# Kernel optimization log

Measured on AMD Instinct MI355X. Metric: run time of the kernel, lower is better.

## Reference

```python
import jax, jax.numpy as jnp
import numpy as np

# DCRNN (PEMS-BAY scale) constants
N = 325      # num_nodes
B = 64       # batch_size
T = 12       # encoder seq_len
HZ = 12      # decoder horizon
U = 64       # rnn_units
DIN = 2      # input_dim
DOUT = 1     # output_dim
K = 2        # max_diffusion_step
NM = K + 1   # num diffusion matrices (Chebyshev, single laplacian support)


def _glorot(key, shape):
    lim = float(np.sqrt(6.0 / (shape[0] + shape[1])))
    return jax.random.uniform(key, shape, jnp.float32, -lim, lim)


def setup_inputs() -> dict:
    key = jax.random.key(0)
    ks = jax.random.split(key, 8)
    # random symmetric adjacency -> scaled Laplacian support (lambda_max ~= 2 approx)
    a = np.asarray(jax.random.uniform(ks[0], (N, N)))
    a = (a + a.T) * 0.5
    a = a * (a > 0.9)
    d = a.sum(1)
    dinv = 1.0 / np.sqrt(np.maximum(d, 1e-8))
    L = np.eye(N, dtype=np.float32) - (dinv[:, None] * a * dinv[None, :]).astype(np.float32)
    support = jnp.asarray(L - np.eye(N, dtype=np.float32))  # 2L/lambda_max - I with lambda_max=2

    def cell_params(k, din):
        f = (din + U) * NM
        k1, k2 = jax.random.split(k)
        return dict(gate_W=_glorot(k1, (f, 2 * U)), gate_b=jnp.zeros((2 * U,), jnp.float32),
                    cand_W=_glorot(k2, (f, U)), cand_b=jnp.zeros((U,), jnp.float32))

    inp = {"inputs": jax.random.normal(ks[1], (T, B, N * DIN), jnp.float32),
           "support": support}
    for name, din, kk in [("enc0", DIN, ks[2]), ("enc1", U, ks[3]),
                          ("dec0", DOUT, ks[4]), ("dec1", U, ks[5])]:
        for pn, v in cell_params(kk, din).items():
            inp[f"{name}_{pn}"] = v
    inp["proj_W"] = _glorot(ks[6], (U, DOUT))
    inp["proj_b"] = jnp.zeros((DOUT,), jnp.float32)
    return inp


def _gconv(x, support, W, b):
    # x: (B, N, F). Chebyshev diffusion: x0=x, x1=Lx, x2=2Lx1-x0, ...
    xs = [x]
    x0, x1 = x, jnp.einsum('mn,bnf->bmf', support, x)
    xs.append(x1)
    for _ in range(2, K + 1):
        x2 = 2.0 * jnp.einsum('mn,bnf->bmf', support, x1) - x0
        xs.append(x2)
        x0, x1 = x1, x2
    xk = jnp.concatenate(xs, axis=-1)  # (B, N, NM*F)
    return xk @ W + b


def _gru_cell(x, h, support, gW, gb, cW, cb):
    # diffusion-conv GRU: r,u gates then candidate
    ru = jax.nn.sigmoid(_gconv(jnp.concatenate([x, h], -1), support, gW, gb))
    r, u = jnp.split(ru, 2, axis=-1)
    c = jnp.tanh(_gconv(jnp.concatenate([x, r * h], -1), support, cW, cb))
    return u * h + (1.0 - u) * c


def reference(inputs, support,
              enc0_gate_W, enc0_gate_b, enc0_cand_W, enc0_cand_b,
              enc1_gate_W, enc1_gate_b, enc1_cand_W, enc1_cand_b,
              dec0_gate_W, dec0_gate_b, dec0_cand_W, dec0_cand_b,
              dec1_gate_W, dec1_gate_b, dec1_cand_W, dec1_cand_b,
              proj_W, proj_b):
    x_seq = inputs.reshape(T, B, N, DIN)
    h0 = jnp.zeros((B, N, U), inputs.dtype)

    def enc_step(carry, x):
        h_l0, h_l1 = carry
        h_l0 = _gru_cell(x, h_l0, support, enc0_gate_W, enc0_gate_b, enc0_cand_W, enc0_cand_b)
        h_l1 = _gru_cell(h_l0, h_l1, support, enc1_gate_W, enc1_gate_b, enc1_cand_W, enc1_cand_b)
        return (h_l0, h_l1), None

    (h_l0, h_l1), _ = jax.lax.scan(enc_step, (h0, h0), x_seq)

    def dec_step(carry, _):
        d_in, hd0, hd1 = carry
        hd0 = _gru_cell(d_in, hd0, support, dec0_gate_W, dec0_gate_b, dec0_cand_W, dec0_cand_b)
        hd1 = _gru_cell(hd0, hd1, support, dec1_gate_W, dec1_gate_b, dec1_cand_W, dec1_cand_b)
        out = hd1 @ proj_W + proj_b  # (B, N, DOUT)
        return (out, hd0, hd1), out.reshape(B, N * DOUT)

    start = jnp.zeros((B, N, DOUT), inputs.dtype)  # GO symbol
    _, outputs = jax.lax.scan(dec_step, (start, h_l0, h_l1), None, length=HZ)
    return outputs  # (horizon, B, N*DOUT)
```

## Files before the change

kernel.cpp:

```cpp
#include <hip/hip_runtime.h>

constexpr int N  = 325;
constexpr int B  = 64;
constexpr int T  = 12;
constexpr int HZ = 12;
constexpr int U  = 64;
constexpr int BN = B * N;

constexpr int SSTIL = 42;
constexpr int SSKC  = 11;
constexpr int XST   = 364;

typedef __attribute__((ext_vector_type(8))) short short8;
typedef __attribute__((ext_vector_type(4))) float floatx4;

__device__ inline unsigned short f2bf(float f) {
    unsigned u = __float_as_uint(f);
    u += 0x7fff + ((u >> 16) & 1);
    return (unsigned short)(u >> 16);
}
__device__ inline unsigned pack_hilo(float v) {
    const unsigned short hi = f2bf(v);
    const float hif = __uint_as_float(((unsigned)hi) << 16);
    const unsigned short lo = f2bf(v - hif);
    return (unsigned)hi | ((unsigned)lo << 16);
}
__device__ inline void unpack8(const uint4 u0, const uint4 u1,
                               short8& h, short8& l) {
    const unsigned uu[8] = {u0.x, u0.y, u0.z, u0.w, u1.x, u1.y, u1.z, u1.w};
    #pragma unroll
    for (int j = 0; j < 8; ++j) {
        h[j] = (short)(uu[j] & 0xffffu);
        l[j] = (short)(uu[j] >> 16);
    }
}


__global__ void zero_kernel(unsigned* __restrict__ p, long n) {
    long i = (long)blockIdx.x * blockDim.x + threadIdx.x;
    const long stride = (long)gridDim.x * blockDim.x;
    for (; i < n; i += stride) p[i] = 0u;
}

__global__ __launch_bounds__(256)
void s2_build(const float* __restrict__ S, float* __restrict__ S2)
{
    const int m = blockIdx.x;
    __shared__ float srow[N];
    for (int i = threadIdx.x; i < N; i += 256) srow[i] = S[m * N + i];
    __syncthreads();
    for (int c = threadIdx.x; c < N; c += 256) {
        float a = 0.f;
        for (int k = 0; k < N; ++k) a += srow[k] * S[k * N + c];
        S2[m * N + c] = a;
    }
}

__global__ __launch_bounds__(64)
void prepack_ss(const float* __restrict__ S, const float* __restrict__ S2,
                short* __restrict__ ssh, short* __restrict__ ssl)
{
    const int t = blockIdx.x, kc = blockIdx.y, lane = threadIdx.x;
    const int quad = lane >> 4, l15 = lane & 15;
    short8 hv, lv;
    #pragma unroll
    for (int j = 0; j < 8; ++j) {
        const int m = t * 16 + l15;
        const int k = kc * 32 + quad * 8 + j;
        float v = 0.f;
        if (k < N) {
            if (m < N) v = S[m * N + k];
            else if (m >= 336 && m < 336 + N) v = S2[(m - 336) * N + k];
        }
        const unsigned short hb = f2bf(v);
        hv[j] = (short)hb;
        lv[j] = (short)f2bf(v - __uint_as_float(((unsigned)hb) << 16));
    }
    const size_t off = ((size_t)(t * SSKC + kc) * 64 + lane);
    ((short8*)ssh)[off] = hv;
    ((short8*)ssl)[off] = lv;
}

__global__ __launch_bounds__(64)
void prepack_w(const float* __restrict__ W, short* __restrict__ Wh,
               short* __restrict__ Wl, int F, int Nout, int NT)
{
    const int kc = blockIdx.x, n = blockIdx.y, lane = threadIdx.x;
    const int quad = lane >> 4, l15 = lane & 15;
    short8 hv, lv;
    #pragma unroll
    for (int j = 0; j < 8; ++j) {
        const int k   = kc * 32 + quad * 8 + j;
        const int col = n * 16 + l15;
        const int lvl = k / F, f = k - lvl * F;
        float w = 0.f;
        if (lvl == 0)
            w = W[(size_t)f * Nout + col] - W[(size_t)(2 * F + f) * Nout + col];
        else if (lvl == 1)
            w = W[(size_t)(F + f) * Nout + col];
        else if (lvl == 2)
            w = 2.f * W[(size_t)(2 * F + f) * Nout + col];
        const unsigned short hb = f2bf(w);
        hv[j] = (short)hb;
        lv[j] = (short)f2bf(w - __uint_as_float(((unsigned)hb) << 16));
    }
    const size_t off = ((size_t)(kc * NT + n) * 64 + lane);
    ((short8*)Wh)[off] = hv;
    ((short8*)Wl)[off] = lv;
}

template<int DIN, int F, int K3P, bool RMUL>
__device__ __forceinline__ void diffuse_body(
    const short8* __restrict__ ssh, const short8* __restrict__ ssl,
    const float* __restrict__ x, const float* __restrict__ h,
    const float* __restrict__ ru, unsigned* __restrict__ zcat,
    int cx, int b, int mh, unsigned* __restrict__ xls)
{
    const int c0 = cx * 32;
    const int tid = threadIdx.x, wave = tid >> 6, lane = tid & 63;
    const int quad = lane >> 4, l15 = lane & 15;

    for (int idx = tid; idx < 352 * 32; idx += 448) {
        const int n = idx >> 5, f = idx & 31, gf = c0 + f;
        unsigned u = 0u;
        if (n < N && gf < F) {
            const int row = b * N + n;
            float v;
            if (gf < DIN) {
                v = x[(size_t)row * DIN + gf];
            } else {
                v = h[(size_t)row * U + (gf - DIN)];
                if (RMUL) v *= ru[(size_t)row * 128 + (gf - DIN)];
            }
            u = pack_hilo(v);
            if (mh == 0 && !(RMUL && gf < DIN))
                zcat[(size_t)row * K3P + gf] = u;
        }
        xls[f * XST + n] = u;
    }
    __syncthreads();

    const int tb = mh * 21 + wave * 3;

    floatx4 acc[3][2];
    #pragma unroll
    for (int i = 0; i < 3; ++i)
        #pragma unroll
        for (int n = 0; n < 2; ++n)
            acc[i][n] = (floatx4){0.f, 0.f, 0.f, 0.f};

    short8 cah[3], cal[3], nah[3], nal[3];
    #pragma unroll
    for (int i = 0; i < 3; ++i) {
        const size_t fo = (size_t)((tb + i) * SSKC) * 64 + lane;
        cah[i] = ssh[fo]; cal[i] = ssl[fo];
    }
    for (int kc = 0; kc < SSKC; ++kc) {
        if (kc + 1 < SSKC) {
            #pragma unroll
            for (int i = 0; i < 3; ++i) {
                const size_t fo = (size_t)((tb + i) * SSKC + kc + 1) * 64 + lane;
                nah[i] = ssh[fo]; nal[i] = ssl[fo];
            }
        }
        short8 bh[2], bl[2];
        const int koff = kc * 32 + quad * 8;
        #pragma unroll
        for (int n = 0; n < 2; ++n) {
            const uint4 u0 = *(const uint4*)&xls[(n * 16 + l15) * XST + koff];
            const uint4 u1 = *(const uint4*)&xls[(n * 16 + l15) * XST + koff + 4];
            unpack8(u0, u1, bh[n], bl[n]);
        }
        #pragma unroll
        for (int i = 0; i < 3; ++i)
            #pragma unroll
            for (int n = 0; n < 2; ++n) {
                acc[i][n] = __builtin_amdgcn_mfma_f32_16x16x32_bf16(cah[i], bh[n], acc[i][n], 0, 0, 0);
                acc[i][n] = __builtin_amdgcn_mfma_f32_16x16x32_bf16(cah[i], bl[n], acc[i][n], 0, 0, 0);
                acc[i][n] = __builtin_amdgcn_mfma_f32_16x16x32_bf16(cal[i], bh[n], acc[i][n], 0, 0, 0);
            }
        if (kc + 1 < SSKC) {
            #pragma unroll
            for (int i = 0; i < 3; ++i) { cah[i] = nah[i]; cal[i] = nal[i]; }
        }
    }

    #pragma unroll
    for (int i = 0; i < 3; ++i) {
        const int t = tb + i;
        #pragma unroll
        for (int n = 0; n < 2; ++n) {
            const int col = c0 + n * 16 + l15;
            if (col >= F) continue;
            #pragma unroll
            for (int r = 0; r < 4; ++r) {
                const int m = t * 16 + quad * 4 + r;
                if (m < N)
                    zcat[(size_t)(b * N + m) * K3P + F + col] = pack_hilo(acc[i][n][r]);
                else if (m >= 336 && m < 336 + N)
                    zcat[(size_t)(b * N + (m - 336)) * K3P + 2 * F + col] = pack_hilo(acc[i][n][r]);
            }
        }
    }
}


__device__ __forceinline__ void gate_body(const unsigned* __restrict__ zcat,
    int K3p, const short8* __restrict__ Wh, const short8* __restrict__ Wl,
    const float* __restrict__ bias, float* __restrict__ ru, int bx, int nb)
{
    constexpr int NT = 4;
    const int tid = threadIdx.x, wave = tid >> 6, lane = tid & 63;
    const int quad = lane >> 4, l15 = lane & 15;
    const int row0 = bx * 64 + wave * 16;

    floatx4 acc[NT];
    #pragma unroll
    for (int n = 0; n < NT; ++n) {
        const float bv = bias[(nb + n) * 16 + l15];
        acc[n] = (floatx4){bv, bv, bv, bv};
    }
    const unsigned* __restrict__ zrow = zcat + (size_t)(row0 + l15) * K3p + quad * 8;
    const int KC = K3p >> 5;
    for (int kc = 0; kc < KC; ++kc) {
        const uint4* p = (const uint4*)(zrow + kc * 32);
        short8 ahi, alo;
        unpack8(p[0], p[1], ahi, alo);
        const short8* __restrict__ wh = Wh + (size_t)(kc * 8 + nb) * 64 + lane;
        const short8* __restrict__ wl = Wl + (size_t)(kc * 8 + nb) * 64 + lane;
        #pragma unroll
        for (int n = 0; n < NT; ++n) {
            const short8 bh = wh[n * 64], bl = wl[n * 64];
            acc[n] = __builtin_amdgcn_mfma_f32_16x16x32_bf16(ahi, bh, acc[n], 0, 0, 0);
            acc[n] = __builtin_amdgcn_mfma_f32_16x16x32_bf16(ahi, bl, acc[n], 0, 0, 0);
            acc[n] = __builtin_amdgcn_mfma_f32_16x16x32_bf16(alo, bh, acc[n], 0, 0, 0);
        }
    }
    #pragma unroll
    for (int n = 0; n < NT; ++n) {
        const int col = (nb + n) * 16 + l15;
        #pragma unroll
        for (int r = 0; r < 4; ++r) {
            const int row = row0 + quad * 4 + r;
            ru[(size_t)row * 128 + col] = 1.f / (1.f + __expf(-acc[n][r]));
        }
    }
}

__device__ __forceinline__ void cand_body(const unsigned* __restrict__ zcat,
    int K3p, const short8* __restrict__ Wh, const short8* __restrict__ Wl,
    const float* __restrict__ bias, const float* __restrict__ ru,
    float* __restrict__ h, int bx, int nb)
{
    constexpr int NT = 2;
    const int tid = threadIdx.x, wave = tid >> 6, lane = tid & 63;
    const int quad = lane >> 4, l15 = lane & 15;
    const int row0 = bx * 64 + wave * 16;

    floatx4 acc[NT];
    #pragma unroll
    for (int n = 0; n < NT; ++n) {
        const float bv = bias[(nb + n) * 16 + l15];
        acc[n] = (floatx4){bv, bv, bv, bv};
    }
    const unsigned* __restrict__ zrow = zcat + (size_t)(row0 + l15) * K3p + quad * 8;
    const int KC = K3p >> 5;
    for (int kc = 0; kc < KC; ++kc) {
        const uint4* p = (const uint4*)(zrow + kc * 32);
        short8 ahi, alo;
        unpack8(p[0], p[1], ahi, alo);
        const short8* __restrict__ wh = Wh + (size_t)(kc * 4 + nb) * 64 + lane;
        const short8* __restrict__ wl = Wl + (size_t)(kc * 4 + nb) * 64 + lane;
        #pragma unroll
        for (int n = 0; n < NT; ++n) {
            const short8 bh = wh[n * 64], bl = wl[n * 64];
            acc[n] = __builtin_amdgcn_mfma_f32_16x16x32_bf16(ahi, bh, acc[n], 0, 0, 0);
            acc[n] = __builtin_amdgcn_mfma_f32_16x16x32_bf16(ahi, bl, acc[n], 0, 0, 0);
            acc[n] = __builtin_amdgcn_mfma_f32_16x16x32_bf16(alo, bh, acc[n], 0, 0, 0);
        }
    }
    #pragma unroll
    for (int n = 0; n < NT; ++n) {
        const int col = (nb + n) * 16 + l15;
        #pragma unroll
        for (int r = 0; r < 4; ++r) {
            const int row = row0 + quad * 4 + r;
            const float c  = tanhf(acc[n][r]);
            const float ug = ru[(size_t)row * 128 + 64 + col];
            const float hv = h[(size_t)row * 64 + col];
            h[(size_t)row * 64 + col] = ug * hv + (1.f - ug) * c;
        }
    }
}


template<int DIN, int F, int K3P, bool RMUL, int CB>
__global__ __launch_bounds__(448, 3)
void diffuse_solo(const short8* __restrict__ ssh, const short8* __restrict__ ssl,
                  const float* __restrict__ x, const float* __restrict__ h,
                  const float* __restrict__ ru, unsigned* __restrict__ zcat)
{
    __shared__ __align__(16) unsigned xls[32 * XST];
    diffuse_body<DIN, F, K3P, RMUL>(ssh, ssl, x, h, ru, zcat,
                                    CB + blockIdx.x, blockIdx.y, blockIdx.z, xls);
}

__global__ __launch_bounds__(256)
void gate_solo(const unsigned* __restrict__ zcat, int K3p,
               const short8* __restrict__ Wh, const short8* __restrict__ Wl,
               const float* __restrict__ bias, float* __restrict__ ru)
{
    gate_body(zcat, K3p, Wh, Wl, bias, ru, blockIdx.x, blockIdx.y * 4);
}

__global__ __launch_bounds__(256)
void cand_solo(const unsigned* __restrict__ zcat, int K3p,
               const short8* __restrict__ Wh, const short8* __restrict__ Wl,
               const float* __restrict__ bias, const float* __restrict__ ru,
               float* __restrict__ h)
{
    cand_body(zcat, K3p, Wh, Wl, bias, ru, h, blockIdx.x, blockIdx.y * 2);
}

__global__ __launch_bounds__(256)
void cand_proj(const unsigned* __restrict__ zcat, int K3p,
               const short8* __restrict__ Wh, const short8* __restrict__ Wl,
               const float* __restrict__ bias, const float* __restrict__ ru,
               float* __restrict__ h, const float* __restrict__ pW,
               const float* __restrict__ pb, float* __restrict__ outp,
               float* __restrict__ dec_in)
{
    constexpr int NT = 4;
    const int tid = threadIdx.x, wave = tid >> 6, lane = tid & 63;
    const int quad = lane >> 4, l15 = lane & 15;
    const int row0 = blockIdx.x * 64 + wave * 16;

    floatx4 acc[NT];
    #pragma unroll
    for (int n = 0; n < NT; ++n) {
        const float bv = bias[n * 16 + l15];
        acc[n] = (floatx4){bv, bv, bv, bv};
    }
    const unsigned* __restrict__ zrow = zcat + (size_t)(row0 + l15) * K3p + quad * 8;
    const int KC = K3p >> 5;
    for (int kc = 0; kc < KC; ++kc) {
        const uint4* p = (const uint4*)(zrow + kc * 32);
        short8 ahi, alo;
        unpack8(p[0], p[1], ahi, alo);
        const short8* __restrict__ wh = Wh + (size_t)(kc * 4) * 64 + lane;
        const short8* __restrict__ wl = Wl + (size_t)(kc * 4) * 64 + lane;
        #pragma unroll
        for (int n = 0; n < NT; ++n) {
            const short8 bh = wh[n * 64], bl = wl[n * 64];
            acc[n] = __builtin_amdgcn_mfma_f32_16x16x32_bf16(ahi, bh, acc[n], 0, 0, 0);
            acc[n] = __builtin_amdgcn_mfma_f32_16x16x32_bf16(ahi, bl, acc[n], 0, 0, 0);
            acc[n] = __builtin_amdgcn_mfma_f32_16x16x32_bf16(alo, bh, acc[n], 0, 0, 0);
        }
    }
    float pr[4] = {0.f, 0.f, 0.f, 0.f};
    #pragma unroll
    for (int n = 0; n < NT; ++n) {
        const int col = n * 16 + l15;
        const float pw = pW[col];
        #pragma unroll
        for (int r = 0; r < 4; ++r) {
            const int row = row0 + quad * 4 + r;
            const float c  = tanhf(acc[n][r]);
            const float ug = ru[(size_t)row * 128 + 64 + col];
            const float hv = h[(size_t)row * 64 + col];
            const float hn = ug * hv + (1.f - ug) * c;
            h[(size_t)row * 64 + col] = hn;
            pr[r] += hn * pw;
        }
    }
    #pragma unroll
    for (int r = 0; r < 4; ++r) {
        float v = pr[r];
        v += __shfl_xor(v, 1); v += __shfl_xor(v, 2);
        v += __shfl_xor(v, 4); v += __shfl_xor(v, 8);
        if (l15 == 0) {
            const int row = row0 + quad * 4 + r;
            const float o = v + pb[0];
            outp[row]   = o;
            dec_in[row] = o;
        }
    }
}


struct DuoDP {
    const short8 *ssh, *ssl;
    const float *xA, *hA, *ruA; unsigned* zA;
    const float *xB, *hB, *ruB; unsigned* zB;
    int cbB;
};

template<bool RM>
__global__ __launch_bounds__(448, 3)
void diffuse_duo(DuoDP P)
{
    __shared__ __align__(16) unsigned xls[32 * XST];
    const int zz = blockIdx.z;
    if (zz < 2) {
        if ((int)blockIdx.x < 3)
            diffuse_body<2, 66, 224, RM>(P.ssh, P.ssl, P.xA, P.hA, P.ruA, P.zA,
                                         blockIdx.x, blockIdx.y, zz, xls);
    } else {
        if ((int)blockIdx.x < 4 - P.cbB)
            diffuse_body<64, 128, 384, RM>(P.ssh, P.ssl, P.xB, P.hB, P.ruB, P.zB,
                                           P.cbB + blockIdx.x, blockIdx.y, zz - 2, xls);
    }
}

struct DuoGP {
    const unsigned* zA; const short8 *WhA, *WlA; const float* bA; float* ruA;
    const unsigned* zB; const short8 *WhB, *WlB; const float* bB; float* ruB;
};

__global__ __launch_bounds__(256)
void gate_duo(DuoGP P)
{
    if (blockIdx.z == 0)
        gate_body(P.zA, 224, P.WhA, P.WlA, P.bA, P.ruA, blockIdx.x, blockIdx.y * 4);
    else
        gate_body(P.zB, 384, P.WhB, P.WlB, P.bB, P.ruB, blockIdx.x, blockIdx.y * 4);
}

struct DuoCP {
    const unsigned* zA; const short8 *WhA, *WlA; const float* bA;
    const float* ruA; float* hA;
    const unsigned* zB; const short8 *WhB, *WlB; const float* bB;
    const float* ruB; float* hB;
};

__global__ __launch_bounds__(256)
void cand_duo(DuoCP P)
{
    if (blockIdx.z == 0)
        cand_body(P.zA, 224, P.WhA, P.WlA, P.bA, P.ruA, P.hA, blockIdx.x, blockIdx.y * 2);
    else
        cand_body(P.zB, 384, P.WhB, P.WlB, P.bB, P.ruB, P.hB, blockIdx.x, blockIdx.y * 2);
}


extern "C" void kernel_launch(void* const* d_in, const int* in_sizes, int n_in,
                              void* d_out, int out_size, void* d_ws, size_t ws_size,
                              hipStream_t stream)
{
    const float* inputs = (const float*)d_in[0];
    const float* S      = (const float*)d_in[1];
    const float* Wt[4][4];
    for (int l = 0; l < 4; ++l)
        for (int j = 0; j < 4; ++j)
            Wt[l][j] = (const float*)d_in[2 + l * 4 + j];
    const float* pW = (const float*)d_in[18];
    const float* pb = (const float*)d_in[19];
    float* out = (float*)d_out;

    float*    ws     = (float*)d_ws;
    float*    h0     = ws;
    float*    h1     = h0 + (size_t)BN * U;
    float*    dec_in = h1 + (size_t)BN * U;
    float*    ruA    = dec_in + BN;
    float*    ruB    = ruA + (size_t)BN * 128;
    unsigned* zcatA  = (unsigned*)(ruB + (size_t)BN * 128);
    unsigned* zcatB  = zcatA + (size_t)BN * 224;
    float*    S2     = (float*)(zcatB + (size_t)BN * 384);
    char*     pp     = (char*)(S2 + (size_t)N * N);
    pp = (char*)(((uintptr_t)pp + 15) & ~(uintptr_t)15);

    short* ssh = (short*)pp;
    short* ssl = ssh + (size_t)SSTIL * SSKC * 64 * 8;
    char*  wpbase = (char*)(ssl + (size_t)SSTIL * SSKC * 64 * 8);

    const int Fs[4]   = {66, 128, 65, 128};
    const int K3ps[4] = {224, 384, 224, 384};
    short *Wgh[4], *Wgl[4], *Wch[4], *Wcl[4];
    size_t off = 0;
    for (int l = 0; l < 4; ++l) {
        const size_t ge = (size_t)K3ps[l] * 128, ce = (size_t)K3ps[l] * 64;
        Wgh[l] = (short*)(wpbase + off); off += ge * 2;
        Wgl[l] = (short*)(wpbase + off); off += ge * 2;
        Wch[l] = (short*)(wpbase + off); off += ce * 2;
        Wcl[l] = (short*)(wpbase + off); off += ce * 2;
    }

    const long zn = (long)BN * (2 * U) + BN + (long)BN * 256 + (long)BN * (224 + 384);
    zero_kernel<<<2048, 256, 0, stream>>>((unsigned*)h0, zn);

    s2_build<<<N, 256, 0, stream>>>(S, S2);
    prepack_ss<<<dim3(SSTIL, SSKC), 64, 0, stream>>>(S, S2, ssh, ssl);
    for (int l = 0; l < 4; ++l) {
        prepack_w<<<dim3(K3ps[l] / 32, 8), 64, 0, stream>>>(Wt[l][0], Wgh[l], Wgl[l],
                                                            Fs[l], 128, 8);
        prepack_w<<<dim3(K3ps[l] / 32, 4), 64, 0, stream>>>(Wt[l][2], Wch[l], Wcl[l],
                                                            Fs[l], 64, 4);
    }

    const short8* SSH = (const short8*)ssh;
    const short8* SSL = (const short8*)ssl;

    for (int s = 0; s <= T; ++s) {
        const float* x0 = inputs + (size_t)s * BN * 2;
        const bool a = (s < T), b1 = (s >= 1);
        if (a && b1) {
            DuoDP dp{SSH, SSL, x0, h0, nullptr, zcatA, h0, h1, nullptr, zcatB, 0};
            diffuse_duo<false><<<dim3(4, B, 4), 448, 0, stream>>>(dp);
            DuoGP gp{zcatA, (short8*)Wgh[0], (short8*)Wgl[0], Wt[0][1], ruA,
                     zcatB, (short8*)Wgh[1], (short8*)Wgl[1], Wt[1][1], ruB};
            gate_duo<<<dim3(BN / 64, 2, 2), 256, 0, stream>>>(gp);
            DuoDP dp2{SSH, SSL, x0, h0, ruA, zcatA, h0, h1, ruB, zcatB, 2};
            diffuse_duo<true><<<dim3(3, B, 4), 448, 0, stream>>>(dp2);
            DuoCP cp{zcatA, (short8*)Wch[0], (short8*)Wcl[0], Wt[0][3], ruA, h0,
                     zcatB, (short8*)Wch[1], (short8*)Wcl[1], Wt[1][3], ruB, h1};
            cand_duo<<<dim3(BN / 64, 2, 2), 256, 0, stream>>>(cp);
        } else if (a) {
            diffuse_solo<2, 66, 224, false, 0><<<dim3(3, B, 2), 448, 0, stream>>>(
                SSH, SSL, x0, h0, nullptr, zcatA);
            gate_solo<<<dim3(BN / 64, 2), 256, 0, stream>>>(
                zcatA, 224, (short8*)Wgh[0], (short8*)Wgl[0], Wt[0][1], ruA);
            diffuse_solo<2, 66, 224, true, 0><<<dim3(3, B, 2), 448, 0, stream>>>(
                SSH, SSL, x0, h0, ruA, zcatA);
            cand_solo<<<dim3(BN / 64, 2), 256, 0, stream>>>(
                zcatA, 224, (short8*)Wch[0], (short8*)Wcl[0], Wt[0][3], ruA, h0);
        } else {
            diffuse_solo<64, 128, 384, false, 0><<<dim3(4, B, 2), 448, 0, stream>>>(
                SSH, SSL, h0, h1, nullptr, zcatB);
            gate_solo<<<dim3(BN / 64, 2), 256, 0, stream>>>(
                zcatB, 384, (short8*)Wgh[1], (short8*)Wgl[1], Wt[1][1], ruB);
            diffuse_solo<64, 128, 384, true, 2><<<dim3(2, B, 2), 448, 0, stream>>>(
                SSH, SSL, h0, h1, ruB, zcatB);
            cand_solo<<<dim3(BN / 64, 2), 256, 0, stream>>>(
                zcatB, 384, (short8*)Wch[1], (short8*)Wcl[1], Wt[1][3], ruB, h1);
        }
    }

    for (int hz = 0; hz < HZ; ++hz) {
        diffuse_solo<1, 65, 224, false, 0><<<dim3(3, B, 2), 448, 0, stream>>>(
            SSH, SSL, dec_in, h0, nullptr, zcatB);
        gate_solo<<<dim3(BN / 64, 2), 256, 0, stream>>>(
            zcatB, 224, (short8*)Wgh[2], (short8*)Wgl[2], Wt[2][1], ruA);
        diffuse_solo<1, 65, 224, true, 0><<<dim3(3, B, 2), 448, 0, stream>>>(
            SSH, SSL, dec_in, h0, ruA, zcatB);
        cand_solo<<<dim3(BN / 64, 2), 256, 0, stream>>>(
            zcatB, 224, (short8*)Wch[2], (short8*)Wcl[2], Wt[2][3], ruA, h0);
        diffuse_solo<64, 128, 384, false, 0><<<dim3(4, B, 2), 448, 0, stream>>>(
            SSH, SSL, h0, h1, nullptr, zcatB);
        gate_solo<<<dim3(BN / 64, 2), 256, 0, stream>>>(
            zcatB, 384, (short8*)Wgh[3], (short8*)Wgl[3], Wt[3][1], ruA);
        diffuse_solo<64, 128, 384, true, 2><<<dim3(2, B, 2), 448, 0, stream>>>(
            SSH, SSL, h0, h1, ruA, zcatB);
        cand_proj<<<BN / 64, 256, 0, stream>>>(
            zcatB, 384, (short8*)Wch[3], (short8*)Wcl[3], Wt[3][3], ruA, h1,
            pW, pb, out + (size_t)hz * BN, dec_in);
    }
}
```

Before: 4.082 ms.

## Merge diffusion row-halves into one 896-thread block and vectorize staging loads

The two blocks that each handled half the output rows of a diffusion tile (blockIdx.z = mh) become one 896-thread block, so the x/h tile is staged into LDS once instead of twice. The duo kernel's grid is flattened so layer-A and layer-B tiles share one x dimension with no idle padded blocks. For the 64-feature layer the staging loop uses float4 loads and uint4 zcat stores. The larger block may limit occupancy and register budget under launch_bounds(896,7).

```diff
diff --git a/kernel.cpp b/kernel.cpp
--- a/kernel.cpp
+++ b/kernel.cpp
@@ -109,38 +109,66 @@
     ((short8*)Wl)[off] = lv;
 }
 
-template<int DIN, int F, int K3P, bool RMUL>
+template<int DIN, int F, int K3P, bool RMUL, bool VEC>
 __device__ __forceinline__ void diffuse_body(
     const short8* __restrict__ ssh, const short8* __restrict__ ssl,
     const float* __restrict__ x, const float* __restrict__ h,
     const float* __restrict__ ru, unsigned* __restrict__ zcat,
-    int cx, int b, int mh, unsigned* __restrict__ xls)
+    int cx, int b, unsigned* __restrict__ xls)
 {
     const int c0 = cx * 32;
     const int tid = threadIdx.x, wave = tid >> 6, lane = tid & 63;
     const int quad = lane >> 4, l15 = lane & 15;
 
-    for (int idx = tid; idx < 352 * 32; idx += 448) {
-        const int n = idx >> 5, f = idx & 31, gf = c0 + f;
-        unsigned u = 0u;
-        if (n < N && gf < F) {
-            const int row = b * N + n;
-            float v;
-            if (gf < DIN) {
-                v = x[(size_t)row * DIN + gf];
-            } else {
-                v = h[(size_t)row * U + (gf - DIN)];
-                if (RMUL) v *= ru[(size_t)row * 128 + (gf - DIN)];
+    if constexpr (VEC) {
+        for (int idx4 = tid; idx4 < 352 * 8; idx4 += 896) {
+            const int n = idx4 >> 3, f = (idx4 & 7) * 4, gf = c0 + f;
+            uint4 pk = make_uint4(0u, 0u, 0u, 0u);
+            if (n < N) {
+                const int row = b * N + n;
+                float4 v;
+                if (gf < DIN) {
+                    v = *(const float4*)&x[(size_t)row * DIN + gf];
+                } else {
+                    v = *(const float4*)&h[(size_t)row * U + (gf - DIN)];
+                    if (RMUL) {
+                        const float4 rv = *(const float4*)&ru[(size_t)row * 128 + (gf - DIN)];
+                        v.x *= rv.x; v.y *= rv.y; v.z *= rv.z; v.w *= rv.w;
+                    }
+                }
+                pk.x = pack_hilo(v.x); pk.y = pack_hilo(v.y);
+                pk.z = pack_hilo(v.z); pk.w = pack_hilo(v.w);
+                if (!(RMUL && gf < DIN))
+                    *(uint4*)&zcat[(size_t)row * K3P + gf] = pk;
             }
-            u = pack_hilo(v);
-            if (mh == 0 && !(RMUL && gf < DIN))
-                zcat[(size_t)row * K3P + gf] = u;
-        }
-        xls[f * XST + n] = u;
+            xls[(f + 0) * XST + n] = pk.x;
+            xls[(f + 1) * XST + n] = pk.y;
+            xls[(f + 2) * XST + n] = pk.z;
+            xls[(f + 3) * XST + n] = pk.w;
+        }
+    } else {
+        for (int idx = tid; idx < 352 * 32; idx += 896) {
+            const int n = idx >> 5, f = idx & 31, gf = c0 + f;
+            unsigned u = 0u;
+            if (n < N && gf < F) {
+                const int row = b * N + n;
+                float v;
+                if (gf < DIN) {
+                    v = x[(size_t)row * DIN + gf];
+                } else {
+                    v = h[(size_t)row * U + (gf - DIN)];
+                    if (RMUL) v *= ru[(size_t)row * 128 + (gf - DIN)];
+                }
+                u = pack_hilo(v);
+                if (!(RMUL && gf < DIN))
+                    zcat[(size_t)row * K3P + gf] = u;
+            }
+            xls[f * XST + n] = u;
+        }
     }
     __syncthreads();
 
-    const int tb = mh * 21 + wave * 3;
+    const int tb = wave * 3;
 
     floatx4 acc[3][2];
     #pragma unroll
@@ -294,15 +322,15 @@
 }
 
 
-template<int DIN, int F, int K3P, bool RMUL, int CB>
-__global__ __launch_bounds__(448, 3)
+template<int DIN, int F, int K3P, bool RMUL, int CB, bool VEC>
+__global__ __launch_bounds__(896, 7)
 void diffuse_solo(const short8* __restrict__ ssh, const short8* __restrict__ ssl,
                   const float* __restrict__ x, const float* __restrict__ h,
                   const float* __restrict__ ru, unsigned* __restrict__ zcat)
 {
     __shared__ __align__(16) unsigned xls[32 * XST];
-    diffuse_body<DIN, F, K3P, RMUL>(ssh, ssl, x, h, ru, zcat,
-                                    CB + blockIdx.x, blockIdx.y, blockIdx.z, xls);
+    diffuse_body<DIN, F, K3P, RMUL, VEC>(ssh, ssl, x, h, ru, zcat,
+                                         CB + blockIdx.x, blockIdx.y, xls);
 }
 
 __global__ __launch_bounds__(256)
@@ -392,24 +420,22 @@
     const short8 *ssh, *ssl;
     const float *xA, *hA, *ruA; unsigned* zA;
     const float *xB, *hB, *ruB; unsigned* zB;
+    int cA;
     int cbB;
 };
 
 template<bool RM>
-__global__ __launch_bounds__(448, 3)
+__global__ __launch_bounds__(896, 7)
 void diffuse_duo(DuoDP P)
 {
     __shared__ __align__(16) unsigned xls[32 * XST];
-    const int zz = blockIdx.z;
-    if (zz < 2) {
-        if ((int)blockIdx.x < 3)
-            diffuse_body<2, 66, 224, RM>(P.ssh, P.ssl, P.xA, P.hA, P.ruA, P.zA,
-                                         blockIdx.x, blockIdx.y, zz, xls);
-    } else {
-        if ((int)blockIdx.x < 4 - P.cbB)
-            diffuse_body<64, 128, 384, RM>(P.ssh, P.ssl, P.xB, P.hB, P.ruB, P.zB,
-                                           P.cbB + blockIdx.x, blockIdx.y, zz - 2, xls);
-    }
+    if ((int)blockIdx.x < P.cA)
+        diffuse_body<2, 66, 224, RM, false>(P.ssh, P.ssl, P.xA, P.hA, P.ruA,
+                                            P.zA, blockIdx.x, blockIdx.y, xls);
+    else
+        diffuse_body<64, 128, 384, RM, true>(P.ssh, P.ssl, P.xB, P.hB, P.ruB,
+                                             P.zB, P.cbB + blockIdx.x - P.cA,
+                                             blockIdx.y, xls);
 }
 
 struct DuoGP {
@@ -504,31 +530,31 @@
         const float* x0 = inputs + (size_t)s * BN * 2;
         const bool a = (s < T), b1 = (s >= 1);
         if (a && b1) {
-            DuoDP dp{SSH, SSL, x0, h0, nullptr, zcatA, h0, h1, nullptr, zcatB, 0};
-            diffuse_duo<false><<<dim3(4, B, 4), 448, 0, stream>>>(dp);
+            DuoDP dp{SSH, SSL, x0, h0, nullptr, zcatA, h0, h1, nullptr, zcatB, 3, 0};
+            diffuse_duo<false><<<dim3(7, B), 896, 0, stream>>>(dp);
             DuoGP gp{zcatA, (short8*)Wgh[0], (short8*)Wgl[0], Wt[0][1], ruA,
                      zcatB, (short8*)Wgh[1], (short8*)Wgl[1], Wt[1][1], ruB};
             gate_duo<<<dim3(BN / 64, 2, 2), 256, 0, stream>>>(gp);
-            DuoDP dp2{SSH, SSL, x0, h0, ruA, zcatA, h0, h1, ruB, zcatB, 2};
-            diffuse_duo<true><<<dim3(3, B, 4), 448, 0, stream>>>(dp2);
+            DuoDP dp2{SSH, SSL, x0, h0, ruA, zcatA, h0, h1, ruB, zcatB, 3, 2};
+            diffuse_duo<true><<<dim3(5, B), 896, 0, stream>>>(dp2);
             DuoCP cp{zcatA, (short8*)Wch[0], (short8*)Wcl[0], Wt[0][3], ruA, h0,
                      zcatB, (short8*)Wch[1], (short8*)Wcl[1], Wt[1][3], ruB, h1};
             cand_duo<<<dim3(BN / 64, 2, 2), 256, 0, stream>>>(cp);
         } else if (a) {
-            diffuse_solo<2, 66, 224, false, 0><<<dim3(3, B, 2), 448, 0, stream>>>(
+            diffuse_solo<2, 66, 224, false, 0, false><<<dim3(3, B), 896, 0, stream>>>(
                 SSH, SSL, x0, h0, nullptr, zcatA);
             gate_solo<<<dim3(BN / 64, 2), 256, 0, stream>>>(
                 zcatA, 224, (short8*)Wgh[0], (short8*)Wgl[0], Wt[0][1], ruA);
-            diffuse_solo<2, 66, 224, true, 0><<<dim3(3, B, 2), 448, 0, stream>>>(
+            diffuse_solo<2, 66, 224, true, 0, false><<<dim3(3, B), 896, 0, stream>>>(
                 SSH, SSL, x0, h0, ruA, zcatA);
             cand_solo<<<dim3(BN / 64, 2), 256, 0, stream>>>(
                 zcatA, 224, (short8*)Wch[0], (short8*)Wcl[0], Wt[0][3], ruA, h0);
         } else {
-            diffuse_solo<64, 128, 384, false, 0><<<dim3(4, B, 2), 448, 0, stream>>>(
+            diffuse_solo<64, 128, 384, false, 0, true><<<dim3(4, B), 896, 0, stream>>>(
                 SSH, SSL, h0, h1, nullptr, zcatB);
             gate_solo<<<dim3(BN / 64, 2), 256, 0, stream>>>(
                 zcatB, 384, (short8*)Wgh[1], (short8*)Wgl[1], Wt[1][1], ruB);
-            diffuse_solo<64, 128, 384, true, 2><<<dim3(2, B, 2), 448, 0, stream>>>(
+            diffuse_solo<64, 128, 384, true, 2, true><<<dim3(2, B), 896, 0, stream>>>(
                 SSH, SSL, h0, h1, ruB, zcatB);
             cand_solo<<<dim3(BN / 64, 2), 256, 0, stream>>>(
                 zcatB, 384, (short8*)Wch[1], (short8*)Wcl[1], Wt[1][3], ruB, h1);
@@ -536,19 +562,19 @@
     }
 
     for (int hz = 0; hz < HZ; ++hz) {
-        diffuse_solo<1, 65, 224, false, 0><<<dim3(3, B, 2), 448, 0, stream>>>(
+        diffuse_solo<1, 65, 224, false, 0, false><<<dim3(3, B), 896, 0, stream>>>(
             SSH, SSL, dec_in, h0, nullptr, zcatB);
         gate_solo<<<dim3(BN / 64, 2), 256, 0, stream>>>(
             zcatB, 224, (short8*)Wgh[2], (short8*)Wgl[2], Wt[2][1], ruA);
-        diffuse_solo<1, 65, 224, true, 0><<<dim3(3, B, 2), 448, 0, stream>>>(
+        diffuse_solo<1, 65, 224, true, 0, false><<<dim3(3, B), 896, 0, stream>>>(
             SSH, SSL, dec_in, h0, ruA, zcatB);
         cand_solo<<<dim3(BN / 64, 2), 256, 0, stream>>>(
             zcatB, 224, (short8*)Wch[2], (short8*)Wcl[2], Wt[2][3], ruA, h0);
-        diffuse_solo<64, 128, 384, false, 0><<<dim3(4, B, 2), 448, 0, stream>>>(
+        diffuse_solo<64, 128, 384, false, 0, true><<<dim3(4, B), 896, 0, stream>>>(
             SSH, SSL, h0, h1, nullptr, zcatB);
         gate_solo<<<dim3(BN / 64, 2), 256, 0, stream>>>(
             zcatB, 384, (short8*)Wgh[3], (short8*)Wgl[3], Wt[3][1], ruA);
-        diffuse_solo<64, 128, 384, true, 2><<<dim3(2, B, 2), 448, 0, stream>>>(
+        diffuse_solo<64, 128, 384, true, 2, true><<<dim3(2, B), 896, 0, stream>>>(
             SSH, SSL, h0, h1, ruA, zcatB);
         cand_proj<<<BN / 64, 256, 0, stream>>>(
             zcatB, 384, (short8*)Wch[3], (short8*)Wcl[3], Wt[3][3], ruA, h1,
```

After: 4.080 ms. Within noise of the previous version (-0.0%).
